# Kernel tuning notes

Measured on AMD Instinct MI355X. Metric: run time of the kernel, lower is better.

## Reference

```python
import jax, jax.numpy as jnp
import numpy as np

B, T, D, H, O = 128, 1024, 256, 512, 128


def _uniform(key, shape, std):
    return jax.random.uniform(key, shape, jnp.float32, -std, std)


def setup_inputs() -> dict:
    key = jax.random.key(0)
    ks = jax.random.split(key, 12)
    std = 1.0 / np.sqrt(H)
    return {
        "x": jax.random.normal(ks[0], (B, T, D), jnp.float32),
        "EC_in": jax.random.normal(ks[1], (B, T, D), jnp.float32),
        "Wx": _uniform(ks[2], (4 * H, D), std),   # x2h weight
        "bx": _uniform(ks[3], (4 * H,), std),
        "Wh": _uniform(ks[4], (4 * H, H), std),   # h2h weight
        "bh": _uniform(ks[5], (4 * H,), std),
        "Wec": _uniform(ks[6], (H, D), std),      # EC weight (dead code in original)
        "bec": _uniform(ks[7], (H,), std),
        "Wfc": _uniform(ks[8], (O, H), std),      # final fc weight
        "bfc": _uniform(ks[9], (O,), std),
    }


def _lstm_forward(x, EC_in, Wx, bx, Wh, bh, Wec, bec, Wfc, bfc):
    # Precompute input projections for all timesteps: [B,T,4H] -> [T,B,4H]
    xg = jnp.einsum("btd,gd->tbg", x, Wx) + bx + bh
    # NOTE: original computes self.EC(EC_in) per step but never uses it (dead code).

    def step(carry, xg_t):
        h, c = carry
        gates = xg_t + h @ Wh.T  # [B, 4H]
        i, f, g, o = jnp.split(gates, 4, axis=1)
        i = jax.nn.sigmoid(i)
        f = jax.nn.sigmoid(f)
        g = jnp.tanh(g)
        o = jax.nn.sigmoid(o)
        c = c * f + i * g
        h = o * jnp.tanh(c)
        return (h, c), None

    h0 = jnp.zeros((x.shape[0], Wh.shape[1]), x.dtype)
    (hT, cT), _ = jax.lax.scan(step, (h0, h0), xg)
    out = hT @ Wfc.T + bfc
    return hT, out


def reference(x, EC_in, Wx, bx, Wh, bh, Wec, bec, Wfc, bfc):
    return _lstm_forward(x, EC_in, Wx, bx, Wh, bh, Wec, bec, Wfc, bfc)
```

## Files before the change

kernel.cpp:

```cpp
#include <hip/hip_runtime.h>

typedef __bf16 bf16;
typedef __bf16 bf16x4 __attribute__((ext_vector_type(4)));
typedef __bf16 bf16x8 __attribute__((ext_vector_type(8)));
typedef float f32x4 __attribute__((ext_vector_type(4)));
typedef unsigned int u32;
typedef unsigned long long u64;

#define T_STEPS 1024
#define BATCH 128
#define DIM 256
#define HID 512
#define NB 128
#define NGRP 8
#define GB 16
#define FLAGS_BYTES 16384

__device__ __forceinline__ f32x4 mfma_bf16(bf16x8 a, bf16x8 b, f32x4 c) {
  return __builtin_amdgcn_mfma_f32_16x16x32_bf16(a, b, c, 0, 0, 0);
}
__device__ __forceinline__ float fast_sigmoid(float v) {
  return __builtin_amdgcn_rcpf(1.f + __expf(-v));
}
__device__ __forceinline__ float fast_tanh(float v) {
  return 2.f * __builtin_amdgcn_rcpf(1.f + __expf(-2.f * v)) - 1.f;
}
__device__ __forceinline__ bf16x8 cvt8(const float* p) {
  float4 a = *(const float4*)p;
  float4 b = *(const float4*)(p + 4);
  bf16x8 r;
  r[0] = (bf16)a.x; r[1] = (bf16)a.y; r[2] = (bf16)a.z; r[3] = (bf16)a.w;
  r[4] = (bf16)b.x; r[5] = (bf16)b.y; r[6] = (bf16)b.z; r[7] = (bf16)b.w;
  return r;
}
__device__ __forceinline__ u32 pack_bf16x2(float a, float b) {
  unsigned short lo = __builtin_bit_cast(unsigned short, (bf16)a);
  unsigned short hi = __builtin_bit_cast(unsigned short, (bf16)b);
  return (u32)lo | ((u32)hi << 16);
}
__device__ __forceinline__ bf16x8 combine(u64 lo, u64 hi) {
  bf16x4 l4 = __builtin_bit_cast(bf16x4, lo);
  bf16x4 h4 = __builtin_bit_cast(bf16x4, hi);
  bf16x8 r;
  r[0] = l4[0]; r[1] = l4[1]; r[2] = l4[2]; r[3] = l4[3];
  r[4] = h4[0]; r[5] = h4[1]; r[6] = h4[2]; r[7] = h4[3];
  return r;
}
__device__ __forceinline__ u64 ld_agent(const u64* p) {
  return __hip_atomic_load(p, __ATOMIC_RELAXED, __HIP_MEMORY_SCOPE_AGENT);
}

__device__ __forceinline__ void wait_group(const u32* flags, int bg, int lane,
                                           u32 target) {
  const int bid_p = ((lane & 15) * NGRP) + bg;
  const u32* my = flags + (size_t)bid_p * 16;
  u32 f = __hip_atomic_load(my, __ATOMIC_RELAXED, __HIP_MEMORY_SCOPE_AGENT);
  while (!__all(f >= target)) {
    __builtin_amdgcn_s_sleep(1);
    f = __hip_atomic_load(my, __ATOMIC_RELAXED, __HIP_MEMORY_SCOPE_AGENT);
  }
}

__device__ __forceinline__ void wait_all128(const u32* flags, int lane, u32 target) {
  const u32* p0 = flags + (size_t)lane * 16;
  const u32* p1 = flags + (size_t)(64 + lane) * 16;
  u32 a = __hip_atomic_load(p0, __ATOMIC_RELAXED, __HIP_MEMORY_SCOPE_AGENT);
  u32 b = __hip_atomic_load(p1, __ATOMIC_RELAXED, __HIP_MEMORY_SCOPE_AGENT);
  while (!__all((a >= target) && (b >= target))) {
    __builtin_amdgcn_s_sleep(1);
    a = __hip_atomic_load(p0, __ATOMIC_RELAXED, __HIP_MEMORY_SCOPE_AGENT);
    b = __hip_atomic_load(p1, __ATOMIC_RELAXED, __HIP_MEMORY_SCOPE_AGENT);
  }
}

__global__ __launch_bounds__(256, 1) void lstm_persist(
    const float* __restrict__ x, const float* __restrict__ Wx,
    const float* __restrict__ bx, const float* __restrict__ Wh,
    const float* __restrict__ bh, const float* __restrict__ Wfc,
    const float* __restrict__ bfc, float* __restrict__ out,
    u32* flags, bf16* hbuf) {
  const int tid = threadIdx.x;
  const int bid = blockIdx.x;
  const int wave = tid >> 6;
  const int lane = tid & 63;
  const int n = lane & 15;
  const int quad = lane >> 4;
  const int sub = n & 3;
  const int bg = bid & 7;
  const int cg = bid >> 3;
  const int mbase = bg * GB;

  __shared__ bf16 lds_h[16][520];

  const int R0 = (n >> 2) * HID + cg * 32 + wave * 8 + sub;
  const int R1 = R0 + 4;
  const float bias0 = bx[R0] + bh[R0];
  const float bias1 = bx[R1] + bh[R1];
  const f32x4 bv0 = {bias0, bias0, bias0, bias0};
  const f32x4 bv1 = {bias1, bias1, bias1, bias1};

  bf16x8 whf0[16], whf1[16];
#pragma unroll
  for (int k = 0; k < 16; ++k) {
    whf0[k] = cvt8(Wh + (size_t)R0 * HID + quad * 8 + k * 32);
    whf1[k] = cvt8(Wh + (size_t)R1 * HID + quad * 8 + k * 32);
  }
  bf16x8 wxf0[8], wxf1[8];
#pragma unroll
  for (int k = 0; k < 8; ++k) {
    wxf0[k] = cvt8(Wx + (size_t)R0 * DIM + quad * 8 + k * 32);
    wxf1[k] = cvt8(Wx + (size_t)R1 * DIM + quad * 8 + k * 32);
  }

  float cst[2][4];
#pragma unroll
  for (int a = 0; a < 2; ++a)
#pragma unroll
    for (int r = 0; r < 4; ++r) cst[a][r] = 0.f;

  const int qb = lane & 48;
  const int srcf = qb | (4 + sub);
  const int srcg = qb | (8 + sub);
  const int srco = qb | (12 + sub);

  const int grow = tid >> 4;
  const int gchunk = tid & 15;

  __syncthreads();

  for (int t = 0; t < T_STEPS; ++t) {
    const bf16* hrd = hbuf + (t & 1) * (BATCH * HID);
    bf16* hwr = hbuf + ((t + 1) & 1) * (BATCH * HID);

    f32x4 acc0 = bv0, acc1 = bv1;

    const float* x0p = x + (size_t)((mbase + n) * 1024 + t) * DIM + quad * 8;
#pragma unroll
    for (int k = 0; k < 8; ++k) {
      bf16x8 A = cvt8(x0p + k * 32);
      acc0 = mfma_bf16(A, wxf0[k], acc0);
      acc1 = mfma_bf16(A, wxf1[k], acc1);
    }

    wait_group(flags, bg, lane, (u32)t);

    {
      const u64* src = (const u64*)hrd + (size_t)(mbase + grow) * (HID / 4) + gchunk * 8;
      u64 hv[8];
#pragma unroll
      for (int j = 0; j < 8; ++j) hv[j] = ld_agent(src + j);
      u64* dst = (u64*)(&lds_h[grow][gchunk * 32]);
#pragma unroll
      for (int j = 0; j < 8; ++j) dst[j] = hv[j];
    }
    __syncthreads();

#pragma unroll
    for (int k = 0; k < 16; ++k) {
      bf16x8 A = *(const bf16x8*)(&lds_h[n][quad * 8 + k * 32]);
      acc0 = mfma_bf16(A, whf0[k], acc0);
      acc1 = mfma_bf16(A, whf1[k], acc1);
    }

    f32x4 accs[2] = {acc0, acc1};
#pragma unroll
    for (int nt = 0; nt < 2; ++nt) {
#pragma unroll
      for (int r = 0; r < 4; ++r) {
        float v = accs[nt][r];
        float s = fast_sigmoid(v);
        float th = fast_tanh(v);
        float pv = (n >= 8 && n < 12) ? th : s;
        float fv = __shfl(pv, srcf, 64);
        float gv = __shfl(pv, srcg, 64);
        float ov = __shfl(pv, srco, 64);
        float cn = cst[nt][r] * fv + pv * gv;
        float hn = ov * fast_tanh(cn);
        cst[nt][r] = cn;
        float h1 = __shfl(hn, qb | 1, 64);
        float h2 = __shfl(hn, qb | 2, 64);
        float h3 = __shfl(hn, qb | 3, 64);
        if (n == 0) {
          int m = mbase + quad * 4 + r;
          int c0 = cg * 32 + wave * 8 + nt * 4;
          u64 pk = (u64)pack_bf16x2(hn, h1) | ((u64)pack_bf16x2(h2, h3) << 32);
          __hip_atomic_store((u64*)(hwr + (size_t)m * HID + c0), pk,
                             __ATOMIC_RELAXED, __HIP_MEMORY_SCOPE_AGENT);
          if (t == T_STEPS - 1) {
            float4 o4 = {hn, h1, h2, h3};
            *(float4*)(out + (size_t)m * HID + c0) = o4;
          }
        }
      }
    }

    __syncthreads();
    if (tid == 0) {
      __hip_atomic_store(flags + (size_t)bid * 16, (u32)(t + 1),
                         __ATOMIC_RELAXED, __HIP_MEMORY_SCOPE_AGENT);
    }
  }

  if (bid < 8) {
    wait_all128(flags, lane, (u32)T_STEPS);
    float* out2 = out + BATCH * HID;
    int col = bid * 16 + n;
    float bcv = bfc[col];
#pragma unroll
    for (int mt = 0; mt < 2; ++mt) {
      int mb = wave * 32 + mt * 16;
      f32x4 a4 = {bcv, bcv, bcv, bcv};
      const u64* ar = (const u64*)hbuf + ((mb + n) * HID) / 4 + quad * 2;
      const float* br = Wfc + col * HID + quad * 8;
#pragma unroll
      for (int k = 0; k < HID; k += 32) {
        bf16x8 A = combine(ld_agent(ar + k / 4), ld_agent(ar + k / 4 + 1));
        bf16x8 B = cvt8(br + k);
        a4 = mfma_bf16(A, B, a4);
      }
#pragma unroll
      for (int r = 0; r < 4; ++r) {
        out2[(mb + quad * 4 + r) * 128 + col] = a4[r];
      }
    }
  }
}

extern "C" void kernel_launch(void* const* d_in, const int* in_sizes, int n_in,
                              void* d_out, int out_size, void* d_ws, size_t ws_size,
                              hipStream_t stream) {
  (void)in_sizes; (void)n_in; (void)out_size; (void)ws_size;
  const float* x   = (const float*)d_in[0];
  const float* Wx  = (const float*)d_in[2];
  const float* bx  = (const float*)d_in[3];
  const float* Wh  = (const float*)d_in[4];
  const float* bh  = (const float*)d_in[5];
  const float* Wfc = (const float*)d_in[8];
  const float* bfc = (const float*)d_in[9];
  float* out = (float*)d_out;
  u32* flags = (u32*)d_ws;
  bf16* hbuf = (bf16*)((char*)d_ws + FLAGS_BYTES);

  hipMemsetAsync(d_ws, 0, FLAGS_BYTES + 2 * BATCH * HID * sizeof(bf16), stream);
  lstm_persist<<<dim3(NB), dim3(256), 0, stream>>>(x, Wx, bx, Wh, bh, Wfc, bfc,
                                                   out, flags, hbuf);
}
```

Measured before the change: 5.805 ms.

## Prefetch next-step x into registers and wait per producer chunk

Loads the next timestep's x row into registers during the current step so the input projection no longer waits on global memory latency. It also replaces the group-wide flag barrier with a per-thread wait on the single producer block whose h chunk the thread copies. Each thread reads its slice of h as soon as that producer is done, instead of waiting for all 16 producers. The cost is extra register pressure (64 floats for x) and a more complex spin loop, and correctness now depends on the remapped grow/gchunk ownership matching producer block ids.

```diff
diff --git a/kernel.cpp b/kernel.cpp
--- a/kernel.cpp
+++ b/kernel.cpp
@@ -33,6 +33,12 @@
   r[4] = (bf16)b.x; r[5] = (bf16)b.y; r[6] = (bf16)b.z; r[7] = (bf16)b.w;
   return r;
 }
+__device__ __forceinline__ bf16x8 cvt8v(float4 a, float4 b) {
+  bf16x8 r;
+  r[0] = (bf16)a.x; r[1] = (bf16)a.y; r[2] = (bf16)a.z; r[3] = (bf16)a.w;
+  r[4] = (bf16)b.x; r[5] = (bf16)b.y; r[6] = (bf16)b.z; r[7] = (bf16)b.w;
+  return r;
+}
 __device__ __forceinline__ u32 pack_bf16x2(float a, float b) {
   unsigned short lo = __builtin_bit_cast(unsigned short, (bf16)a);
   unsigned short hi = __builtin_bit_cast(unsigned short, (bf16)b);
@@ -48,17 +54,6 @@
 }
 __device__ __forceinline__ u64 ld_agent(const u64* p) {
   return __hip_atomic_load(p, __ATOMIC_RELAXED, __HIP_MEMORY_SCOPE_AGENT);
-}
-
-__device__ __forceinline__ void wait_group(const u32* flags, int bg, int lane,
-                                           u32 target) {
-  const int bid_p = ((lane & 15) * NGRP) + bg;
-  const u32* my = flags + (size_t)bid_p * 16;
-  u32 f = __hip_atomic_load(my, __ATOMIC_RELAXED, __HIP_MEMORY_SCOPE_AGENT);
-  while (!__all(f >= target)) {
-    __builtin_amdgcn_s_sleep(1);
-    f = __hip_atomic_load(my, __ATOMIC_RELAXED, __HIP_MEMORY_SCOPE_AGENT);
-  }
 }
 
 __device__ __forceinline__ void wait_all128(const u32* flags, int lane, u32 target) {
@@ -123,8 +118,17 @@
   const int srcg = qb | (8 + sub);
   const int srco = qb | (12 + sub);
 
-  const int grow = tid >> 4;
-  const int gchunk = tid & 15;
+  const int grow = tid & 15;
+  const int gchunk = tid >> 4;
+  const u32* prodflag = flags + (size_t)(((gchunk << 3) | bg) * 16);
+
+  const float* xrow = x + (size_t)(mbase + n) * 1024 * DIM + quad * 8;
+  float4 xa[8], xb[8];
+#pragma unroll
+  for (int k = 0; k < 8; ++k) {
+    xa[k] = *(const float4*)(xrow + k * 32);
+    xb[k] = *(const float4*)(xrow + k * 32 + 4);
+  }
 
   __syncthreads();
 
@@ -134,21 +138,39 @@
 
     f32x4 acc0 = bv0, acc1 = bv1;
 
-    const float* x0p = x + (size_t)((mbase + n) * 1024 + t) * DIM + quad * 8;
 #pragma unroll
     for (int k = 0; k < 8; ++k) {
-      bf16x8 A = cvt8(x0p + k * 32);
+      bf16x8 A = cvt8v(xa[k], xb[k]);
       acc0 = mfma_bf16(A, wxf0[k], acc0);
       acc1 = mfma_bf16(A, wxf1[k], acc1);
     }
 
-    wait_group(flags, bg, lane, (u32)t);
+    {
+      const int tp = (t + 1 < T_STEPS) ? t + 1 : t;
+      const float* xp = xrow + (size_t)tp * DIM;
+#pragma unroll
+      for (int k = 0; k < 8; ++k) {
+        xa[k] = *(const float4*)(xp + k * 32);
+        xb[k] = *(const float4*)(xp + k * 32 + 4);
+      }
+    }
 
     {
       const u64* src = (const u64*)hrd + (size_t)(mbase + grow) * (HID / 4) + gchunk * 8;
       u64 hv[8];
-#pragma unroll
-      for (int j = 0; j < 8; ++j) hv[j] = ld_agent(src + j);
+      bool done = false;
+      while (true) {
+        if (!done) {
+          u32 f = __hip_atomic_load(prodflag, __ATOMIC_RELAXED, __HIP_MEMORY_SCOPE_AGENT);
+          if (f >= (u32)t) {
+#pragma unroll
+            for (int j = 0; j < 8; ++j) hv[j] = ld_agent(src + j);
+            done = true;
+          }
+        }
+        if (__all(done)) break;
+        __builtin_amdgcn_s_sleep(1);
+      }
       u64* dst = (u64*)(&lds_h[grow][gchunk * 32]);
 #pragma unroll
       for (int j = 0; j < 8; ++j) dst[j] = hv[j];
```

Result: slower. 6.007 ms (+3.5%).
